# Performance work log

Hardware: AMD Instinct MI355X
Metric: run time of the kernel (lower is better)

Reference implementation:

```python
import jax, jax.numpy as jnp
import numpy as np

DIM = 1024
HID = 4096
NH = 16
HD = DIM // NH
B, S = 4, 2048
EPS = 1e-5
NEG = -1e9  # stand-in for -inf causal mask fill (numerically safe)


def layer_norm(x, g, b):
    mu = jnp.mean(x, axis=-1, keepdims=True)
    var = jnp.mean((x - mu) ** 2, axis=-1, keepdims=True)
    return (x - mu) * jax.lax.rsqrt(var + EPS) * g + b


def setup_inputs() -> dict:
    key = jax.random.key(0)
    ks = jax.random.split(key, 8)
    x = jax.random.normal(ks[0], (B, S, DIM), dtype=jnp.float32)
    # causal additive mask, broadcastable to [B, NH, S, S]
    causal = jnp.tril(jnp.ones((S, S), dtype=bool))
    mask = jnp.where(causal, 0.0, NEG).astype(jnp.float32)[None, None]
    sc = 1.0 / np.sqrt(DIM)
    wq = jax.random.normal(ks[1], (DIM, DIM), dtype=jnp.float32) * sc
    wk = jax.random.normal(ks[2], (DIM, DIM), dtype=jnp.float32) * sc
    wv = jax.random.normal(ks[3], (DIM, DIM), dtype=jnp.float32) * sc
    wo = jax.random.normal(ks[4], (DIM, DIM), dtype=jnp.float32) * sc
    w1 = jax.random.normal(ks[5], (DIM, HID), dtype=jnp.float32) * sc
    w2 = jax.random.normal(ks[6], (HID, DIM), dtype=jnp.float32) * (1.0 / np.sqrt(HID))
    ln1_w = jnp.ones((DIM,), jnp.float32); ln1_b = jnp.zeros((DIM,), jnp.float32)
    ln2_w = jnp.ones((DIM,), jnp.float32); ln2_b = jnp.zeros((DIM,), jnp.float32)
    return {"x": x, "mask": mask, "wq": wq, "wk": wk, "wv": wv, "wo": wo,
            "w1": w1, "w2": w2, "ln1_w": ln1_w, "ln1_b": ln1_b,
            "ln2_w": ln2_w, "ln2_b": ln2_b}


def reference(x, mask, wq, wk, wv, wo, w1, w2, ln1_w, ln1_b, ln2_w, ln2_b):
    b, s, _ = x.shape
    # pre-norm attention
    xn = layer_norm(x, ln1_w, ln1_b)
    q = (xn @ wq).reshape(b, s, NH, HD)
    k = (xn @ wk).reshape(b, s, NH, HD)
    v = (xn @ wv).reshape(b, s, NH, HD)
    scores = jnp.einsum('bqhd,bkhd->bhqk', q, k) / np.sqrt(HD) + mask
    probs = jax.nn.softmax(scores.astype(jnp.float32), axis=-1).astype(x.dtype)
    attn = jnp.einsum('bhqk,bkhd->bqhd', probs, v).reshape(b, s, NH * HD)
    h = x + attn @ wo
    # pre-norm ReLU FFN
    hn = layer_norm(h, ln2_w, ln2_b)
    ff = jax.nn.relu((hn @ w1).astype(jnp.float32)).astype(x.dtype) @ w2
    return h + ff
```

## Files before the change

kernel.cpp:

```cpp
#include <hip/hip_runtime.h>
#include <hip/hip_bf16.h>
#include <type_traits>

#define DIM 1024
#define HID 4096
#define NH 16
#define HD 64
#define BB 4
#define SS 2048
#define NROW (BB*SS)

typedef __attribute__((ext_vector_type(8))) short short8;
typedef __attribute__((ext_vector_type(4))) short short4v;
typedef __attribute__((ext_vector_type(4))) float f32x4;

__device__ __forceinline__ void gload16(const void* src, void* lds) {
  __builtin_amdgcn_global_load_lds(
      (const __attribute__((address_space(1))) unsigned int*)src,
      (__attribute__((address_space(3))) unsigned int*)lds, 16, 0, 0);
}
__device__ __forceinline__ short f2b(float f) {
  return __builtin_bit_cast(short, __float2bfloat16(f));
}
__device__ __forceinline__ float b2f(short s) {
  return __uint_as_float(((unsigned)(unsigned short)s) << 16);
}

__global__ __launch_bounds__(256) void ln_k(const float* __restrict__ x,
                                            const float* __restrict__ g,
                                            const float* __restrict__ bta,
                                            short* __restrict__ out) {
  int row = blockIdx.x;
  int t = threadIdx.x;
  int lane = t & 63, wid = t >> 6;
  float4 v = *(const float4*)(x + (size_t)row*DIM + t*4);
  float f[4] = {v.x, v.y, v.z, v.w};
  float s1 = 0.f, s2 = 0.f;
#pragma unroll
  for (int j = 0; j < 4; j++) { s1 += f[j]; s2 += f[j]*f[j]; }
#pragma unroll
  for (int off = 32; off > 0; off >>= 1) { s1 += __shfl_xor(s1, off); s2 += __shfl_xor(s2, off); }
  __shared__ float red[8];
  if (lane == 0) { red[wid] = s1; red[4+wid] = s2; }
  __syncthreads();
  s1 = red[0]+red[1]+red[2]+red[3];
  s2 = red[4]+red[5]+red[6]+red[7];
  float mu = s1 * (1.0f/DIM);
  float var = s2 * (1.0f/DIM) - mu*mu;
  float rs = rsqrtf(var + 1e-5f);
  float4 gv = *(const float4*)(g + t*4);
  float4 bv = *(const float4*)(bta + t*4);
  short4v o;
  o[0] = f2b((f[0]-mu)*rs*gv.x + bv.x);
  o[1] = f2b((f[1]-mu)*rs*gv.y + bv.y);
  o[2] = f2b((f[2]-mu)*rs*gv.z + bv.z);
  o[3] = f2b((f[3]-mu)*rs*gv.w + bv.w);
  *(short4v*)(out + (size_t)row*DIM + t*4) = o;
}

__global__ __launch_bounds__(256) void transp_f2b(const float* __restrict__ in, short* __restrict__ out,
                                                  int R, int C) {
  __shared__ __align__(16) short tile[64][72];
  int r0 = blockIdx.x*64, c0 = blockIdx.y*64;
  int t = threadIdx.x;
  int cr = t >> 4;
  int cc4 = (t & 15) * 4;
#pragma unroll
  for (int i = 0; i < 4; i++) {
    float4 v = *(const float4*)(in + (size_t)(r0 + cr + i*16)*C + c0 + cc4);
    tile[cr + i*16][cc4 + 0] = f2b(v.x);
    tile[cr + i*16][cc4 + 1] = f2b(v.y);
    tile[cr + i*16][cc4 + 2] = f2b(v.z);
    tile[cr + i*16][cc4 + 3] = f2b(v.w);
  }
  __syncthreads();
  int rr = t >> 3, cc = (t & 7) * 8;
#pragma unroll
  for (int i = 0; i < 2; i++) {
    int oc = rr + i*32;
    short8 v;
#pragma unroll
    for (int j = 0; j < 8; j++) v[j] = tile[cc + j][oc];
    *(short8*)(out + (size_t)(c0 + oc)*R + r0 + cc) = v;
  }
}

__global__ __launch_bounds__(256) void transp_f2b4(const float* __restrict__ w0, const float* __restrict__ w1,
                                                   const float* __restrict__ w2, const float* __restrict__ w3,
                                                   short* __restrict__ o0, short* __restrict__ o1,
                                                   short* __restrict__ o2, short* __restrict__ o3) {
  __shared__ __align__(16) short tile[64][72];
  int zz = blockIdx.z;
  const float* in = (zz == 0) ? w0 : (zz == 1) ? w1 : (zz == 2) ? w2 : w3;
  short* out = (zz == 0) ? o0 : (zz == 1) ? o1 : (zz == 2) ? o2 : o3;
  const int R = DIM, C = DIM;
  int r0 = blockIdx.x*64, c0 = blockIdx.y*64;
  int t = threadIdx.x;
  int cr = t >> 4;
  int cc4 = (t & 15) * 4;
#pragma unroll
  for (int i = 0; i < 4; i++) {
    float4 v = *(const float4*)(in + (size_t)(r0 + cr + i*16)*C + c0 + cc4);
    tile[cr + i*16][cc4 + 0] = f2b(v.x);
    tile[cr + i*16][cc4 + 1] = f2b(v.y);
    tile[cr + i*16][cc4 + 2] = f2b(v.z);
    tile[cr + i*16][cc4 + 3] = f2b(v.w);
  }
  __syncthreads();
  int rr = t >> 3, cc = (t & 7) * 8;
#pragma unroll
  for (int i = 0; i < 2; i++) {
    int oc = rr + i*32;
    short8 v;
#pragma unroll
    for (int j = 0; j < 8; j++) v[j] = tile[cc + j][oc];
    *(short8*)(out + (size_t)(c0 + oc)*R + r0 + cc) = v;
  }
}

__global__ __launch_bounds__(256) void vtrans(const short* __restrict__ qkv, short* __restrict__ vt) {
  __shared__ __align__(16) short tile[64][72];
  int s0 = blockIdx.x*64;
  int z = blockIdx.y; int b = z >> 4, h = z & 15;
  int t = threadIdx.x;
  int rr = t >> 3, cc = (t & 7) * 8;
#pragma unroll
  for (int i = 0; i < 2; i++) {
    short8 v = *(const short8*)(qkv + (size_t)(b*SS + s0 + rr + i*32)*(3*DIM) + 2*DIM + h*HD + cc);
    *(short8*)&tile[rr + i*32][cc] = v;
  }
  __syncthreads();
#pragma unroll
  for (int i = 0; i < 2; i++) {
    int d = rr + i*32;
    short8 v;
#pragma unroll
    for (int j = 0; j < 8; j++) v[j] = tile[cc + j][d];
    *(short8*)(vt + ((size_t)z*HD + d)*SS + s0 + cc) = v;
  }
}

template<int EPI, typename CT>
__global__ __launch_bounds__(512) void gemm_bt(const short* __restrict__ A, int lda,
                                               const short* __restrict__ Bt, int ldb,
                                               CT* C, int ldc,
                                               const float* Res, int ldr,
                                               int K) {
  __shared__ __align__(16) short ldsA[128*128];
  __shared__ __align__(16) short ldsB[128*128];
  int t = threadIdx.x, lane = t & 63, wid = t >> 6;
  int bm = blockIdx.x*128, bn = blockIdx.y*128;
  int wr = wid >> 2, wc = wid & 3;
  f32x4 z4 = {0.f, 0.f, 0.f, 0.f};
  f32x4 acc[4][2];
#pragma unroll
  for (int m = 0; m < 4; m++)
#pragma unroll
    for (int n = 0; n < 2; n++) acc[m][n] = z4;
  const int srcCol = (((t & 15) ^ ((t >> 4) & 15)) * 8);
  const short* pa = A + (size_t)(bm + (t >> 4))*lda + srcCol;
  const short* pb = Bt + (size_t)(bn + (t >> 4))*ldb + srcCol;
  const int rdXor = (lane & 15) << 3;
  for (int k0 = 0; k0 < K; k0 += 128) {
#pragma unroll
    for (int i = 0; i < 4; i++) {
      gload16(pa + (size_t)(i*32)*lda, &ldsA[i*4096 + wid*512]);
      gload16(pb + (size_t)(i*32)*ldb, &ldsB[i*4096 + wid*512]);
    }
    pa += 128; pb += 128;
    __syncthreads();
#pragma unroll
    for (int kk = 0; kk < 4; kk++) {
      short8 af[4], bfr[2];
#pragma unroll
      for (int m = 0; m < 4; m++) {
        int row = wr*64 + m*16 + (lane & 15);
        af[m] = *(const short8*)&ldsA[row*128 + ((kk*32 + (lane >> 4)*8) ^ rdXor)];
      }
#pragma unroll
      for (int n = 0; n < 2; n++) {
        int row = wc*32 + n*16 + (lane & 15);
        bfr[n] = *(const short8*)&ldsB[row*128 + ((kk*32 + (lane >> 4)*8) ^ rdXor)];
      }
#pragma unroll
      for (int m = 0; m < 4; m++)
#pragma unroll
        for (int n = 0; n < 2; n++)
          acc[m][n] = __builtin_amdgcn_mfma_f32_16x16x32_bf16(af[m], bfr[n], acc[m][n], 0, 0, 0);
    }
    __syncthreads();
  }
#pragma unroll
  for (int m = 0; m < 4; m++) {
    int r0 = bm + wr*64 + m*16 + ((lane >> 4) << 2);
#pragma unroll
    for (int n = 0; n < 2; n++) {
      int c = bn + wc*32 + n*16 + (lane & 15);
#pragma unroll
      for (int r = 0; r < 4; r++) {
        float v = acc[m][n][r];
        if constexpr (EPI == 1) v = fmaxf(v, 0.0f);
        if constexpr (EPI == 3) v += Res[(size_t)(r0 + r)*ldr + c];
        if constexpr (std::is_same<CT, float>::value)
          C[(size_t)(r0 + r)*ldc + c] = v;
        else
          C[(size_t)(r0 + r)*ldc + c] = f2b(v);
      }
    }
  }
}

__global__ __launch_bounds__(512) void attn_k(short* qkv, const short* __restrict__ vt) {
  __shared__ __align__(16) short ldsK[2][64*64];
  __shared__ __align__(16) short ldsV[2][64*64];
  __shared__ __align__(16) short ldsP[8][16*64];
  int t = threadIdx.x, lane = t & 63, wid = t >> 6;
  int wgid = blockIdx.x;
  int xcd = wgid & 7, idx = wgid >> 3;
  int z  = xcd*8 + (idx & 7);
  int qi = 15 - (idx >> 3);
  int q0 = qi*128;
  int b = z >> 4, h = z & 15;
  const int ld = 3*DIM;
  const float SCALE2 = 0.125f * 1.44269504f;
  const float THR2   = 8.0f * 1.44269504f;
  const int half = wid >> 2;
  const int myq = q0 + wid*16;
  short8 qf[2];
  {
    const short* qp = qkv + (size_t)(b*SS + myq + (lane & 15))*ld + h*HD + (lane >> 4)*8;
    qf[0] = *(const short8*)qp;
    qf[1] = *(const short8*)(qp + 32);
  }
  f32x4 z4 = {0.f, 0.f, 0.f, 0.f};
  f32x4 accO[4];
#pragma unroll
  for (int n = 0; n < 4; n++) accO[n] = z4;
  float m_r[4], lp[4];
#pragma unroll
  for (int r = 0; r < 4; r++) { m_r[r] = -1e30f; lp[r] = 0.f; }
  const int srcCol = (((lane & 7) ^ ((lane >> 3) & 7)) * 8);
  const int rowXor = (lane & 7) << 3;
  int ntiles = 2*qi + 2;

  auto STAGE = [&](int it, int bsel) {
    int kv0 = it*64;
    const short* sk = qkv + (size_t)(b*SS + kv0 + (t >> 3))*ld + DIM + h*HD + srcCol;
    gload16(sk, &ldsK[bsel][wid*512]);
    const short* sv = vt + ((size_t)z*HD + (t >> 3))*SS + kv0 + srcCol;
    gload16(sv, &ldsV[bsel][wid*512]);
  };

  STAGE(0, 0);
  __syncthreads();
  for (int it = 0; it < ntiles; ++it) {
    int cur = it & 1;
    if (it + 1 < ntiles) STAGE(it + 1, cur ^ 1);
    int kv0 = it*64;
    if (it <= 2*qi + half) {
      f32x4 sacc[4];
#pragma unroll
      for (int n = 0; n < 4; n++) sacc[n] = z4;
      __builtin_amdgcn_s_setprio(1);
#pragma unroll
      for (int n = 0; n < 4; n++) {
#pragma unroll
        for (int kk = 0; kk < 2; kk++) {
          int colK = (kk*32 + (lane >> 4)*8) ^ rowXor;
          short8 kb = *(const short8*)&ldsK[cur][(n*16 + (lane & 15))*64 + colK];
          sacc[n] = __builtin_amdgcn_mfma_f32_16x16x32_bf16(qf[kk], kb, sacc[n], 0, 0, 0);
        }
      }
      __builtin_amdgcn_s_setprio(0);
      if (it == 2*qi + half) {
#pragma unroll
        for (int n = 0; n < 4; n++) {
          int kg = kv0 + n*16 + (lane & 15);
#pragma unroll
          for (int r = 0; r < 4; r++) {
            int qg = myq + ((lane >> 4) << 2) + r;
            sacc[n][r] = (kg <= qg) ? sacc[n][r] : -1e30f;
          }
        }
      }
      float mxs[4];
      float dmax = -1e30f;
#pragma unroll
      for (int r = 0; r < 4; r++) {
        float mx = fmaxf(fmaxf(sacc[0][r], sacc[1][r]), fmaxf(sacc[2][r], sacc[3][r]));
#pragma unroll
        for (int off = 1; off < 16; off <<= 1) mx = fmaxf(mx, __shfl_xor(mx, off));
        mxs[r] = mx * SCALE2;
        dmax = fmaxf(dmax, mxs[r] - m_r[r]);
      }
      if (__any(dmax > THR2)) {
#pragma unroll
        for (int r = 0; r < 4; r++) {
          float mn = fmaxf(m_r[r], mxs[r]);
          float al = exp2f(m_r[r] - mn);
          m_r[r] = mn;
          lp[r] *= al;
#pragma unroll
          for (int n = 0; n < 4; n++) accO[n][r] *= al;
        }
      }
#pragma unroll
      for (int r = 0; r < 4; r++) {
        float mn = m_r[r];
        float rs = 0.f;
#pragma unroll
        for (int n = 0; n < 4; n++) {
          float p = exp2f(fmaf(sacc[n][r], SCALE2, -mn));
          sacc[n][r] = p;
          rs += p;
        }
        lp[r] += rs;
      }
#pragma unroll
      for (int n = 0; n < 4; n++)
#pragma unroll
        for (int r = 0; r < 4; r++) {
          int prow = ((lane >> 4) << 2) + r;
          int pcol = (n*16 + (lane & 15)) ^ ((prow & 7) << 3);
          ldsP[wid][prow*64 + pcol] = f2b(sacc[n][r]);
        }
      __builtin_amdgcn_s_setprio(1);
#pragma unroll
      for (int nn = 0; nn < 4; nn++) {
#pragma unroll
        for (int kk = 0; kk < 2; kk++) {
          int colP = (kk*32 + (lane >> 4)*8) ^ rowXor;
          short8 vb  = *(const short8*)&ldsV[cur][(nn*16 + (lane & 15))*64 + colP];
          short8 pfr = *(const short8*)&ldsP[wid][(lane & 15)*64 + colP];
          accO[nn] = __builtin_amdgcn_mfma_f32_16x16x32_bf16(pfr, vb, accO[nn], 0, 0, 0);
        }
      }
      __builtin_amdgcn_s_setprio(0);
    }
    __syncthreads();
  }
  {
    float rl[4];
#pragma unroll
    for (int r = 0; r < 4; r++) {
      float l = lp[r];
#pragma unroll
      for (int off = 1; off < 16; off <<= 1) l += __shfl_xor(l, off);
      rl[r] = 1.0f / l;
    }
#pragma unroll
    for (int nn = 0; nn < 4; nn++) {
#pragma unroll
      for (int r = 0; r < 4; r++) {
        int qg = myq + ((lane >> 4) << 2) + r;
        float ov = accO[nn][r] * rl[r];
        qkv[(size_t)(b*SS + qg)*ld + 2*DIM + h*HD + nn*16 + (lane & 15)] = f2b(ov);
      }
    }
  }
}

extern "C" void kernel_launch(void* const* d_in, const int* in_sizes, int n_in,
                              void* d_out, int out_size, void* d_ws, size_t ws_size,
                              hipStream_t stream) {
  (void)in_sizes; (void)n_in; (void)out_size; (void)ws_size;
  const float* x    = (const float*)d_in[0];
  const float* wq   = (const float*)d_in[2];
  const float* wk   = (const float*)d_in[3];
  const float* wv   = (const float*)d_in[4];
  const float* wo   = (const float*)d_in[5];
  const float* w1   = (const float*)d_in[6];
  const float* w2   = (const float*)d_in[7];
  const float* ln1w = (const float*)d_in[8];
  const float* ln1b = (const float*)d_in[9];
  const float* ln2w = (const float*)d_in[10];
  const float* ln2b = (const float*)d_in[11];
  float* out = (float*)d_out;

  short* ws = (short*)d_ws;
  size_t o = 0;
  short* wqkvT = ws + o; o += (size_t)3*DIM*DIM;
  short* woT   = ws + o; o += (size_t)DIM*DIM;
  short* w1T   = ws + o; o += (size_t)HID*DIM;
  short* w2T   = ws + o; o += (size_t)DIM*HID;
  short* xn    = ws + o; o += (size_t)NROW*DIM;
  short* qkv   = ws + o; o += (size_t)NROW*3*DIM;
  short* ff1   = ws + o; o += (size_t)NROW*HID;
  short* vtb   = ff1;

  dim3 B256(256), B512(512);
  transp_f2b4<<<dim3(16,16,4), B256, 0, stream>>>(wq, wk, wv, wo,
                                                  wqkvT, wqkvT + DIM*DIM, wqkvT + 2*DIM*DIM, woT);
  transp_f2b<<<dim3(16,64), B256, 0, stream>>>(w1, w1T, DIM, HID);
  transp_f2b<<<dim3(64,16), B256, 0, stream>>>(w2, w2T, HID, DIM);
  ln_k<<<NROW, B256, 0, stream>>>(x, ln1w, ln1b, xn);
  gemm_bt<0, short><<<dim3(NROW/128, 3*DIM/128), B512, 0, stream>>>(xn, DIM, wqkvT, DIM, qkv, 3*DIM, nullptr, 0, DIM);
  vtrans<<<dim3(SS/64, BB*NH), B256, 0, stream>>>(qkv, vtb);
  attn_k<<<dim3(1024), B512, 0, stream>>>(qkv, vtb);
  gemm_bt<3, float><<<dim3(NROW/128, DIM/128), B512, 0, stream>>>(qkv + 2*DIM, 3*DIM, woT, DIM, out, DIM, x, DIM, DIM);
  ln_k<<<NROW, B256, 0, stream>>>(out, ln2w, ln2b, xn);
  gemm_bt<1, short><<<dim3(NROW/128, HID/128), B512, 0, stream>>>(xn, DIM, w1T, DIM, ff1, HID, nullptr, 0, DIM);
  gemm_bt<3, float><<<dim3(NROW/128, DIM/128), B512, 0, stream>>>(ff1, HID, w2T, HID, out, DIM, out, DIM, HID);
}
```

Baseline: 388.3 us.

## Pair complementary causal query tiles per attention workgroup for balanced work

Each attention workgroup now processes two query tiles, qi and 15-qi, one after the other, so every block walks a constant 34 KV tiles instead of a varying 2*qi+2. The grid is halved to 512 blocks, and the KV staging pipeline continues across the tile switch, with an epilogue and state reset in between. This targets the tail imbalance of causal attention, where blocks with late query tiles do far more work. In exchange there are fewer blocks to hide latency and some added index arithmetic per iteration.

```diff
diff --git a/kernel.cpp b/kernel.cpp
--- a/kernel.cpp
+++ b/kernel.cpp
@@ -218,44 +218,76 @@
   int wgid = blockIdx.x;
   int xcd = wgid & 7, idx = wgid >> 3;
   int z  = xcd*8 + (idx & 7);
-  int qi = 15 - (idx >> 3);
-  int q0 = qi*128;
+  int p  = idx >> 3;
+  int qiA = 15 - p, qiB = p;
   int b = z >> 4, h = z & 15;
   const int ld = 3*DIM;
   const float SCALE2 = 0.125f * 1.44269504f;
   const float THR2   = 8.0f * 1.44269504f;
   const int half = wid >> 2;
-  const int myq = q0 + wid*16;
+  const int nA = 2*qiA + 2;
+  const int NT = 34;
+
   short8 qf[2];
-  {
-    const short* qp = qkv + (size_t)(b*SS + myq + (lane & 15))*ld + h*HD + (lane >> 4)*8;
+  f32x4 z4 = {0.f, 0.f, 0.f, 0.f};
+  f32x4 accO[4];
+  float m_r[4], lp[4];
+  const int srcCol = (((lane & 7) ^ ((lane >> 3) & 7)) * 8);
+  const int rowXor = (lane & 7) << 3;
+
+  auto LOADQ = [&](int q0) {
+    const short* qp = qkv + (size_t)(b*SS + q0 + wid*16 + (lane & 15))*ld + h*HD + (lane >> 4)*8;
     qf[0] = *(const short8*)qp;
     qf[1] = *(const short8*)(qp + 32);
-  }
-  f32x4 z4 = {0.f, 0.f, 0.f, 0.f};
-  f32x4 accO[4];
-#pragma unroll
-  for (int n = 0; n < 4; n++) accO[n] = z4;
-  float m_r[4], lp[4];
-#pragma unroll
-  for (int r = 0; r < 4; r++) { m_r[r] = -1e30f; lp[r] = 0.f; }
-  const int srcCol = (((lane & 7) ^ ((lane >> 3) & 7)) * 8);
-  const int rowXor = (lane & 7) << 3;
-  int ntiles = 2*qi + 2;
-
-  auto STAGE = [&](int it, int bsel) {
-    int kv0 = it*64;
+  };
+  auto RESET = [&]() {
+#pragma unroll
+    for (int n = 0; n < 4; n++) accO[n] = z4;
+#pragma unroll
+    for (int r = 0; r < 4; r++) { m_r[r] = -1e30f; lp[r] = 0.f; }
+  };
+  auto EPILOG = [&](int q0e) {
+    float rl[4];
+#pragma unroll
+    for (int r = 0; r < 4; r++) {
+      float l = lp[r];
+#pragma unroll
+      for (int off = 1; off < 16; off <<= 1) l += __shfl_xor(l, off);
+      rl[r] = 1.0f / l;
+    }
+#pragma unroll
+    for (int nn = 0; nn < 4; nn++)
+#pragma unroll
+      for (int r = 0; r < 4; r++) {
+        int qg = q0e + wid*16 + ((lane >> 4) << 2) + r;
+        qkv[(size_t)(b*SS + qg)*ld + 2*DIM + h*HD + nn*16 + (lane & 15)] = f2b(accO[nn][r] * rl[r]);
+      }
+  };
+  auto STAGE = [&](int kv0, int bsel) {
     const short* sk = qkv + (size_t)(b*SS + kv0 + (t >> 3))*ld + DIM + h*HD + srcCol;
     gload16(sk, &ldsK[bsel][wid*512]);
     const short* sv = vt + ((size_t)z*HD + (t >> 3))*SS + kv0 + srcCol;
     gload16(sv, &ldsV[bsel][wid*512]);
   };
 
+  LOADQ(qiA*128);
+  RESET();
+  int qi = qiA, q0 = qiA*128;
   STAGE(0, 0);
   __syncthreads();
-  for (int it = 0; it < ntiles; ++it) {
-    int cur = it & 1;
-    if (it + 1 < ntiles) STAGE(it + 1, cur ^ 1);
+  for (int v = 0; v < NT; ++v) {
+    int cur = v & 1;
+    if (v + 1 < NT) {
+      int vn = v + 1;
+      STAGE(((vn >= nA) ? vn - nA : vn) * 64, cur ^ 1);
+    }
+    if (v == nA) {
+      EPILOG(q0);
+      RESET();
+      qi = qiB; q0 = qiB*128;
+      LOADQ(q0);
+    }
+    int it = (v >= nA) ? v - nA : v;
     int kv0 = it*64;
     if (it <= 2*qi + half) {
       f32x4 sacc[4];
@@ -278,7 +310,7 @@
           int kg = kv0 + n*16 + (lane & 15);
 #pragma unroll
           for (int r = 0; r < 4; r++) {
-            int qg = myq + ((lane >> 4) << 2) + r;
+            int qg = q0 + wid*16 + ((lane >> 4) << 2) + r;
             sacc[n][r] = (kg <= qg) ? sacc[n][r] : -1e30f;
           }
         }
@@ -310,9 +342,9 @@
         float rs = 0.f;
 #pragma unroll
         for (int n = 0; n < 4; n++) {
-          float p = exp2f(fmaf(sacc[n][r], SCALE2, -mn));
-          sacc[n][r] = p;
-          rs += p;
+          float p2 = exp2f(fmaf(sacc[n][r], SCALE2, -mn));
+          sacc[n][r] = p2;
+          rs += p2;
         }
         lp[r] += rs;
       }
@@ -339,25 +371,7 @@
     }
     __syncthreads();
   }
-  {
-    float rl[4];
-#pragma unroll
-    for (int r = 0; r < 4; r++) {
-      float l = lp[r];
-#pragma unroll
-      for (int off = 1; off < 16; off <<= 1) l += __shfl_xor(l, off);
-      rl[r] = 1.0f / l;
-    }
-#pragma unroll
-    for (int nn = 0; nn < 4; nn++) {
-#pragma unroll
-      for (int r = 0; r < 4; r++) {
-        int qg = myq + ((lane >> 4) << 2) + r;
-        float ov = accO[nn][r] * rl[r];
-        qkv[(size_t)(b*SS + qg)*ld + 2*DIM + h*HD + nn*16 + (lane & 15)] = f2b(ov);
-      }
-    }
-  }
+  EPILOG(q0);
 }
 
 extern "C" void kernel_launch(void* const* d_in, const int* in_sizes, int n_in,
@@ -396,7 +410,7 @@
   ln_k<<<NROW, B256, 0, stream>>>(x, ln1w, ln1b, xn);
   gemm_bt<0, short><<<dim3(NROW/128, 3*DIM/128), B512, 0, stream>>>(xn, DIM, wqkvT, DIM, qkv, 3*DIM, nullptr, 0, DIM);
   vtrans<<<dim3(SS/64, BB*NH), B256, 0, stream>>>(qkv, vtb);
-  attn_k<<<dim3(1024), B512, 0, stream>>>(qkv, vtb);
+  attn_k<<<dim3(512), B512, 0, stream>>>(qkv, vtb);
   gemm_bt<3, float><<<dim3(NROW/128, DIM/128), B512, 0, stream>>>(qkv + 2*DIM, 3*DIM, woT, DIM, out, DIM, x, DIM, DIM);
   ln_k<<<NROW, B256, 0, stream>>>(out, ln2w, ln2b, xn);
   gemm_bt<1, short><<<dim3(NROW/128, HID/128), B512, 0, stream>>>(xn, DIM, w1T, DIM, ff1, HID, nullptr, 0, DIM);
```

Result: no change. 385.0 us (-0.9%).
